# Performance work log

Measured on AMD Instinct MI355X. Metric: run time of the kernel, lower is better.

The kernel has to match this reference:

```python
import jax, jax.numpy as jnp
import numpy as np

EPS = 1e-5

def _bn(x, w, b, rm, rv):
    # eval-mode BatchNorm over channel axis (x: [..., C] broadcastable)
    return (x - rm) * (w * jax.lax.rsqrt(rv + EPS)) + b

def setup_inputs() -> dict:
    key = jax.random.key(0)
    ks = jax.random.split(key, 20)
    B, C, H, W = 2, 64, 96, 96
    Cq = C // 8  # query/key channels
    Cr = C // 8  # SE reduction channels
    s = 0.05
    inp = {
        'x': jax.random.normal(ks[0], (B, C, H, W), jnp.float32),
        'wq': jax.random.normal(ks[1], (Cq, C), jnp.float32) * s,
        'bq': jnp.zeros((Cq,), jnp.float32),
        'wk': jax.random.normal(ks[2], (Cq, C), jnp.float32) * s,
        'bk': jnp.zeros((Cq,), jnp.float32),
        'wv': jax.random.normal(ks[3], (C, C), jnp.float32) * s,
        'bv': jnp.zeros((C,), jnp.float32),
        'gamma': jnp.full((1,), 0.5, jnp.float32),
        'bn_w': jnp.ones((C,), jnp.float32),
        'bn_b': jnp.zeros((C,), jnp.float32),
        'bn_rm': jax.random.normal(ks[4], (C,), jnp.float32) * 0.1,
        'bn_rv': jax.random.uniform(ks[5], (C,), jnp.float32) + 0.5,
        'se_w1': jax.random.normal(ks[6], (Cr, C), jnp.float32) * s,
        'se_b1': jnp.zeros((Cr,), jnp.float32),
        'se_bn1_w': jnp.ones((Cr,), jnp.float32),
        'se_bn1_b': jnp.zeros((Cr,), jnp.float32),
        'se_bn1_rm': jax.random.normal(ks[7], (Cr,), jnp.float32) * 0.1,
        'se_bn1_rv': jax.random.uniform(ks[8], (Cr,), jnp.float32) + 0.5,
        'se_w2': jax.random.normal(ks[9], (C, Cr), jnp.float32) * s,
        'se_b2': jnp.zeros((C,), jnp.float32),
        'se_bn2_w': jnp.ones((C,), jnp.float32),
        'se_bn2_b': jnp.zeros((C,), jnp.float32),
        'se_bn2_rm': jax.random.normal(ks[10], (C,), jnp.float32) * 0.1,
        'se_bn2_rv': jax.random.uniform(ks[11], (C,), jnp.float32) + 0.5,
    }
    return inp

def reference(x, wq, bq, wk, bk, wv, bv, gamma, bn_w, bn_b, bn_rm, bn_rv,
              se_w1, se_b1, se_bn1_w, se_bn1_b, se_bn1_rm, se_bn1_rv,
              se_w2, se_b2, se_bn2_w, se_bn2_b, se_bn2_rm, se_bn2_rv):
    B, C, H, W = x.shape
    N = H * W
    xf = x.reshape(B, C, N)
    # PAM branch: 1x1 conv projections
    q = jnp.einsum('oc,bcn->bno', wq, xf) + bq            # [B,N,C/8]
    k = jnp.einsum('oc,bcn->bon', wk, xf) + bk[:, None]    # [B,C/8,N]
    v = jnp.einsum('oc,bcn->bon', wv, xf) + bv[:, None]    # [B,C,N]
    energy = jnp.einsum('bno,bom->bnm', q, k)              # [B,N,N]
    attn = jax.nn.softmax(energy, axis=-1)
    # out[b,c,i] = sum_j v[b,c,j] * attn[b,i,j]  (bmm(V, attn^T))
    out = jnp.einsum('bcj,bij->bci', v, attn)
    out = gamma[0] * out
    out = _bn(out, bn_w[:, None], bn_b[:, None], bn_rm[:, None], bn_rv[:, None])
    pam = out.reshape(B, C, H, W)
    # SE branch: GAP + 1x1 conv-bn-relu x2, multiplicative gate
    a = xf.mean(axis=2)                                    # [B,C]
    a1 = jax.nn.relu(_bn(a @ se_w1.T + se_b1, se_bn1_w, se_bn1_b, se_bn1_rm, se_bn1_rv))
    a2 = jax.nn.relu(_bn(a1 @ se_w2.T + se_b2, se_bn2_w, se_bn2_b, se_bn2_rm, se_bn2_rv))
    se = x * a2[:, :, None, None]
    return x + se + pam
```

## Files before the change

### kernel.cpp

```cpp
#include <hip/hip_runtime.h>
#include <hip/hip_bf16.h>

#define B_SZ   2
#define C_CH   64
#define NQ     8
#define NPIX   9216
#define NJC    288
#define QBLKS  288
#define KPART  4
#define KEYS_P 2304
#define NCHUNK 36
#define SM_F   2080
#define NP4    2304

typedef short bf16x8 __attribute__((ext_vector_type(8)));
typedef float f32x4  __attribute__((ext_vector_type(4)));
typedef unsigned u32x4 __attribute__((ext_vector_type(4)));
typedef unsigned uint2v __attribute__((ext_vector_type(2)));

static __device__ __forceinline__ unsigned pack2bf(float a, float b){
    union { __hip_bfloat16 h; unsigned short us; } ca, cb;
    ca.h = __float2bfloat16(a); cb.h = __float2bfloat16(b);
    return (unsigned)ca.us | ((unsigned)cb.us << 16);
}

static __device__ __forceinline__ unsigned short bf16b(float a){
    union { __hip_bfloat16 h; unsigned short us; } c;
    c.h = __float2bfloat16(a); return c.us;
}

__global__ __launch_bounds__(256) void prep_kernel(
    const float* __restrict__ x,
    const float* __restrict__ wq, const float* __restrict__ bq,
    const float* __restrict__ wk, const float* __restrict__ bk,
    const float* __restrict__ wv, const float* __restrict__ bv,
    __hip_bfloat16* __restrict__ qp, __hip_bfloat16* __restrict__ kp,
    __hip_bfloat16* __restrict__ vswz, float* __restrict__ amean)
{
    const int blk = blockIdx.x, tid = threadIdx.x;
    if (blk < 144){
        int t  = blk*256 + tid;
        int n  = (t % NP4) * 4;
        int c8 = (t / NP4) & 7;
        int b  = t / (NP4*8);
        c8 = __builtin_amdgcn_readfirstlane(c8);
        b  = __builtin_amdgcn_readfirstlane(b);
        float acc[8][4];
#pragma unroll
        for (int k = 0; k < 8; ++k){
            float bvv = bv[c8*8 + k];
            acc[k][0] = bvv; acc[k][1] = bvv; acc[k][2] = bvv; acc[k][3] = bvv;
        }
#pragma unroll 4
        for (int ci = 0; ci < C_CH; ++ci){
            const float4 xv = *reinterpret_cast<const float4*>(
                x + (size_t)(b*C_CH + ci)*NPIX + n);
#pragma unroll
            for (int k = 0; k < 8; ++k){
                float w = wv[(c8*8 + k)*C_CH + ci];
                acc[k][0] = fmaf(xv.x, w, acc[k][0]);
                acc[k][1] = fmaf(xv.y, w, acc[k][1]);
                acc[k][2] = fmaf(xv.z, w, acc[k][2]);
                acc[k][3] = fmaf(xv.w, w, acc[k][3]);
            }
        }
#pragma unroll
        for (int k = 0; k < 8; ++k){
            int c = c8*8 + k;
            size_t base = ((size_t)((b*NJC + (n >> 5))*4 + (c >> 4)))*512
                        + ((c & 15)*32) + (n & 31);
            unsigned long long wpk =
                (unsigned long long)pack2bf(acc[k][0], acc[k][1]) |
                ((unsigned long long)pack2bf(acc[k][2], acc[k][3]) << 32);
            *reinterpret_cast<unsigned long long*>(vswz + base) = wpk;
        }
    } else if (blk < 180){
        int t  = (blk - 144)*256 + tid;
        int n  = (t % NP4) * 4;
        int o8 = (t / NP4) & 1;
        int b  = t / (NP4*2);
        o8 = __builtin_amdgcn_readfirstlane(o8);
        b  = __builtin_amdgcn_readfirstlane(b);
        const bool isq = (o8 == 0);
        const float* w    = isq ? wq : wk;
        const float* bias = isq ? bq : bk;
        float acc[8][4];
#pragma unroll
        for (int k = 0; k < 8; ++k){
            float bb = bias[k];
            acc[k][0] = bb; acc[k][1] = bb; acc[k][2] = bb; acc[k][3] = bb;
        }
#pragma unroll 4
        for (int ci = 0; ci < C_CH; ++ci){
            const float4 xv = *reinterpret_cast<const float4*>(
                x + (size_t)(b*C_CH + ci)*NPIX + n);
#pragma unroll
            for (int k = 0; k < 8; ++k){
                float wv_ = w[k*C_CH + ci];
                acc[k][0] = fmaf(xv.x, wv_, acc[k][0]);
                acc[k][1] = fmaf(xv.y, wv_, acc[k][1]);
                acc[k][2] = fmaf(xv.z, wv_, acc[k][2]);
                acc[k][3] = fmaf(xv.w, wv_, acc[k][3]);
            }
        }
        if (isq){
#pragma unroll
            for (int k = 0; k < 8; ++k)
#pragma unroll
                for (int px = 0; px < 4; ++px) acc[k][px] *= 1.44269504f;
        }
        __hip_bfloat16* dst = isq ? qp : kp;
#pragma unroll
        for (int px = 0; px < 4; ++px){
            bf16x8 row;
#pragma unroll
            for (int k = 0; k < 8; ++k) row[k] = (short)bf16b(acc[k][px]);
            *reinterpret_cast<bf16x8*>(dst + ((size_t)(b*NPIX + n + px))*NQ) = row;
        }
    } else {
        int bc = blk - 180;
        float s = 0.f;
        for (int i = tid; i < NPIX; i += 256) s += x[(size_t)bc*NPIX + i];
#pragma unroll
        for (int o = 32; o > 0; o >>= 1) s += __shfl_down(s, o, 64);
        __shared__ float red[4];
        if ((tid & 63) == 0) red[tid >> 6] = s;
        __syncthreads();
        if (tid == 0) amean[bc] = (red[0] + red[1] + red[2] + red[3]) * (1.f / (float)NPIX);
    }
}

__global__ __launch_bounds__(256, 4) void flash_fused(
    const __hip_bfloat16* __restrict__ qp,
    const __hip_bfloat16* __restrict__ kp,
    const __hip_bfloat16* __restrict__ vswz,
    const float* __restrict__ amean,
    const float* __restrict__ sw1, const float* __restrict__ sb1,
    const float* __restrict__ s1w, const float* __restrict__ s1b,
    const float* __restrict__ s1m, const float* __restrict__ s1v,
    const float* __restrict__ sw2, const float* __restrict__ sb2,
    const float* __restrict__ s2w, const float* __restrict__ s2b,
    const float* __restrict__ s2m, const float* __restrict__ s2v,
    const float* __restrict__ x,
    const float* __restrict__ gamma,
    const float* __restrict__ bnw, const float* __restrict__ bnb,
    const float* __restrict__ bnm, const float* __restrict__ bnv,
    float* __restrict__ out)
{
    __shared__ __align__(16) float sm[KPART*SM_F];

    const int qt2 = blockIdx.x, b = blockIdx.y;
    const int p  = threadIdx.x >> 6;
    const int l  = threadIdx.x & 63;
    const int lq = l & 15;
    const int lg = l >> 4;
    const int vlane = lq*32 + lg*8;

    float a1r;
    {
        int r8 = l & 7;
        float s = sb1[r8];
#pragma unroll 8
        for (int c = 0; c < C_CH; ++c)
            s = fmaf(amean[b*C_CH + c], sw1[r8*C_CH + c], s);
        s = (s - s1m[r8]) * (s1w[r8] * rsqrtf(s1v[r8] + 1e-5f)) + s1b[r8];
        a1r = fmaxf(s, 0.f);
    }

    bf16x8 zf = {0,0,0,0,0,0,0,0};
    bf16x8 qfrag[2];
#pragma unroll
    for (int qi = 0; qi < 2; ++qi){
        qfrag[qi] = zf;
        if (lg == 0)
            qfrag[qi] = *reinterpret_cast<const bf16x8*>(
                qp + (size_t)(b*NPIX + qt2*32 + qi*16 + lq) * NQ);
    }

    bf16x8 ones;
#pragma unroll
    for (int i = 0; i < 8; ++i) ones[i] = (short)0x3F80;

    f32x4 Of[2][4];
#pragma unroll
    for (int qi = 0; qi < 2; ++qi)
#pragma unroll
        for (int i = 0; i < 4; ++i) Of[qi][i] = (f32x4){0.f, 0.f, 0.f, 0.f};
    f32x4 Lf[2];
    Lf[0] = (f32x4){0.f, 0.f, 0.f, 0.f};
    Lf[1] = (f32x4){0.f, 0.f, 0.f, 0.f};

    for (int ch = 0; ch < NCHUNK; ++ch){
        const int j0  = p*KEYS_P + ch*64;
        const int jcb = b*NJC + (j0 >> 5);

        bf16x8 kf[4];
#pragma unroll
        for (int jt = 0; jt < 4; ++jt){
            kf[jt] = zf;
            if (lg == 0)
                kf[jt] = *reinterpret_cast<const bf16x8*>(kp + (size_t)(b*NPIX + j0 + jt*16 + lq) * NQ);
        }
        bf16x8 vf[2][4];
#pragma unroll
        for (int kc = 0; kc < 2; ++kc)
#pragma unroll
            for (int ct = 0; ct < 4; ++ct)
                vf[kc][ct] = *reinterpret_cast<const bf16x8*>(
                    vswz + ((size_t)((jcb + kc)*4 + ct))*512 + vlane);

#pragma unroll
        for (int qi = 0; qi < 2; ++qi){
            f32x4 Sf[4];
#pragma unroll
            for (int jt = 0; jt < 4; ++jt)
                Sf[jt] = __builtin_amdgcn_mfma_f32_16x16x32_bf16(kf[jt], qfrag[qi], (f32x4){0.f,0.f,0.f,0.f}, 0, 0, 0);

            unsigned D[4][2];
#pragma unroll
            for (int jt = 0; jt < 4; ++jt){
                D[jt][0] = pack2bf(exp2f(Sf[jt][0]), exp2f(Sf[jt][1]));
                D[jt][1] = pack2bf(exp2f(Sf[jt][2]), exp2f(Sf[jt][3]));
            }

#pragma unroll
            for (int kc = 0; kc < 2; ++kc){
                unsigned o0, o1, o2, o3;
                {
                    uint2v r1 = __builtin_amdgcn_permlane32_swap(D[2*kc][0], D[2*kc+1][0], false, false);
                    uint2v r2 = __builtin_amdgcn_permlane16_swap(r1[0], r1[1], false, false);
                    o0 = r2[0]; o2 = r2[1];
                }
                {
                    uint2v r1 = __builtin_amdgcn_permlane32_swap(D[2*kc][1], D[2*kc+1][1], false, false);
                    uint2v r2 = __builtin_amdgcn_permlane16_swap(r1[0], r1[1], false, false);
                    o1 = r2[0]; o3 = r2[1];
                }
                u32x4 pu; pu[0] = o0; pu[1] = o1; pu[2] = o2; pu[3] = o3;
                bf16x8 pf = __builtin_bit_cast(bf16x8, pu);
#pragma unroll
                for (int ct = 0; ct < 4; ++ct)
                    Of[qi][ct] = __builtin_amdgcn_mfma_f32_16x16x32_bf16(vf[kc][ct], pf, Of[qi][ct], 0, 0, 0);
                Lf[qi] = __builtin_amdgcn_mfma_f32_16x16x32_bf16(ones, pf, Lf[qi], 0, 0, 0);
            }
        }
    }

#pragma unroll
    for (int qi = 0; qi < 2; ++qi)
#pragma unroll
        for (int ct = 0; ct < 4; ++ct)
#pragma unroll
            for (int r = 0; r < 4; ++r)
                sm[p*SM_F + qi*1024 + (ct*4 + r)*64 + l] = Of[qi][ct][r];
    if (l < 16){
        sm[p*SM_F + 2048 + lq]      = Lf[0][0];
        sm[p*SM_F + 2048 + 16 + lq] = Lf[1][0];
    }
    __syncthreads();

    {
        const int ct = threadIdx.x >> 6;
        float gam = gamma[0];

        float a1g[8];
#pragma unroll
        for (int j = 0; j < 8; ++j) a1g[j] = __shfl(a1r, (l & 56) | j, 64);
        float a2v[4];
#pragma unroll
        for (int r = 0; r < 4; ++r){
            int c = ct*16 + lg*4 + r;
            float s = sb2[c];
#pragma unroll
            for (int j = 0; j < 8; ++j) s = fmaf(a1g[j], sw2[c*NQ + j], s);
            s = (s - s2m[c]) * (s2w[c] * rsqrtf(s2v[c] + 1e-5f)) + s2b[c];
            a2v[r] = fmaxf(s, 0.f);
        }

#pragma unroll
        for (int qi = 0; qi < 2; ++qi){
            float L = 0.f;
#pragma unroll
            for (int q = 0; q < KPART; ++q) L += sm[q*SM_F + 2048 + qi*16 + lq];
            float invL = 1.f / L;
            int n = qt2*32 + qi*16 + lq;
#pragma unroll
            for (int r = 0; r < 4; ++r){
                float O = 0.f;
#pragma unroll
                for (int q = 0; q < KPART; ++q) O += sm[q*SM_F + qi*1024 + (ct*4 + r)*64 + l];
                int c = ct*16 + lg*4 + r;
                float pam = gam * O * invL;
                pam = (pam - bnm[c]) * (bnw[c] * rsqrtf(bnv[c] + 1e-5f)) + bnb[c];
                float xv = x[(size_t)(b*C_CH + c)*NPIX + n];
                out[(size_t)(b*C_CH + c)*NPIX + n] = fmaf(xv, a2v[r], xv + pam);
            }
        }
    }
}

extern "C" void kernel_launch(void* const* d_in, const int* in_sizes, int n_in,
                              void* d_out, int out_size, void* d_ws, size_t ws_size,
                              hipStream_t stream)
{
    const float* x     = (const float*)d_in[0];
    const float* wq    = (const float*)d_in[1];
    const float* bq    = (const float*)d_in[2];
    const float* wk    = (const float*)d_in[3];
    const float* bk    = (const float*)d_in[4];
    const float* wv    = (const float*)d_in[5];
    const float* bv    = (const float*)d_in[6];
    const float* gamma = (const float*)d_in[7];
    const float* bnw   = (const float*)d_in[8];
    const float* bnb   = (const float*)d_in[9];
    const float* bnm   = (const float*)d_in[10];
    const float* bnv   = (const float*)d_in[11];
    const float* sw1   = (const float*)d_in[12];
    const float* sb1   = (const float*)d_in[13];
    const float* s1w   = (const float*)d_in[14];
    const float* s1b   = (const float*)d_in[15];
    const float* s1m   = (const float*)d_in[16];
    const float* s1v   = (const float*)d_in[17];
    const float* sw2   = (const float*)d_in[18];
    const float* sb2   = (const float*)d_in[19];
    const float* s2w   = (const float*)d_in[20];
    const float* s2b   = (const float*)d_in[21];
    const float* s2m   = (const float*)d_in[22];
    const float* s2v   = (const float*)d_in[23];

    size_t off = 0;
    auto give = [&](size_t bytes) -> void* {
        void* r = (char*)d_ws + off;
        off += (bytes + 255) & ~(size_t)255;
        return r;
    };
    __hip_bfloat16* qp   = (__hip_bfloat16*)give((size_t)B_SZ*NPIX*NQ*2);
    __hip_bfloat16* kp   = (__hip_bfloat16*)give((size_t)B_SZ*NPIX*NQ*2);
    __hip_bfloat16* vswz = (__hip_bfloat16*)give((size_t)B_SZ*C_CH*NPIX*2);
    float* amean = (float*)give((size_t)B_SZ*C_CH*4);

    prep_kernel<<<dim3(308), dim3(256), 0, stream>>>(x, wq, bq, wk, bk, wv, bv,
                                                     qp, kp, vswz, amean);
    flash_fused<<<dim3(QBLKS, B_SZ), dim3(256), 0, stream>>>(
        qp, kp, vswz, amean,
        sw1, sb1, s1w, s1b, s1m, s1v,
        sw2, sb2, s2w, s2b, s2m, s2v,
        x, gamma, bnw, bnb, bnm, bnv, (float*)d_out);
}
```

Before: 212.9 us.

## Split keys across eight waves per block with two-stage LDS reduction

Doubles the waves per flash block from four to eight, so each wave handles half as many keys (1152 instead of 2304). The partial O and L accumulators are combined in two steps: the upper four waves write to shared memory, then the lower four add into it. This keeps the shared-memory footprint at four slices. The epilogue is re-split so each of the eight waves handles one (query half, channel tile) pair. The aim is more latency hiding and shorter per-wave serial chains, at the cost of an extra barrier and an LDS read-modify-write. Launch bounds of 512x4 may also constrain registers and cause spills.

```diff
diff --git a/kernel.cpp b/kernel.cpp
--- a/kernel.cpp
+++ b/kernel.cpp
@@ -7,9 +7,9 @@
 #define NPIX   9216
 #define NJC    288
 #define QBLKS  288
-#define KPART  4
-#define KEYS_P 2304
-#define NCHUNK 36
+#define KPART  8
+#define KEYS_P 1152
+#define NCHUNK 18
 #define SM_F   2080
 #define NP4    2304
 
@@ -130,7 +130,7 @@
     }
 }
 
-__global__ __launch_bounds__(256, 4) void flash_fused(
+__global__ __launch_bounds__(512, 4) void flash_fused(
     const __hip_bfloat16* __restrict__ qp,
     const __hip_bfloat16* __restrict__ kp,
     const __hip_bfloat16* __restrict__ vswz,
@@ -147,7 +147,7 @@
     const float* __restrict__ bnm, const float* __restrict__ bnv,
     float* __restrict__ out)
 {
-    __shared__ __align__(16) float sm[KPART*SM_F];
+    __shared__ __align__(16) float sm[4*SM_F];
 
     const int qt2 = blockIdx.x, b = blockIdx.y;
     const int p  = threadIdx.x >> 6;
@@ -246,21 +246,40 @@
         }
     }
 
-#pragma unroll
-    for (int qi = 0; qi < 2; ++qi)
-#pragma unroll
-        for (int ct = 0; ct < 4; ++ct)
-#pragma unroll
-            for (int r = 0; r < 4; ++r)
-                sm[p*SM_F + qi*1024 + (ct*4 + r)*64 + l] = Of[qi][ct][r];
-    if (l < 16){
-        sm[p*SM_F + 2048 + lq]      = Lf[0][0];
-        sm[p*SM_F + 2048 + 16 + lq] = Lf[1][0];
+    if (p >= 4){
+        const int ps = p - 4;
+#pragma unroll
+        for (int qi = 0; qi < 2; ++qi)
+#pragma unroll
+            for (int ct = 0; ct < 4; ++ct)
+#pragma unroll
+                for (int r = 0; r < 4; ++r)
+                    sm[ps*SM_F + qi*1024 + (ct*4 + r)*64 + l] = Of[qi][ct][r];
+        if (l < 16){
+            sm[ps*SM_F + 2048 + lq]      = Lf[0][0];
+            sm[ps*SM_F + 2048 + 16 + lq] = Lf[1][0];
+        }
     }
     __syncthreads();
+    if (p < 4){
+#pragma unroll
+        for (int qi = 0; qi < 2; ++qi)
+#pragma unroll
+            for (int ct = 0; ct < 4; ++ct)
+#pragma unroll
+                for (int r = 0; r < 4; ++r)
+                    sm[p*SM_F + qi*1024 + (ct*4 + r)*64 + l] += Of[qi][ct][r];
+        if (l < 16){
+            sm[p*SM_F + 2048 + lq]      += Lf[0][0];
+            sm[p*SM_F + 2048 + 16 + lq] += Lf[1][0];
+        }
+    }
+    __syncthreads();
 
     {
-        const int ct = threadIdx.x >> 6;
+        const int w8 = threadIdx.x >> 6;
+        const int qi = w8 >> 2;
+        const int ct = w8 & 3;
         float gam = gamma[0];
 
         float a1g[8];
@@ -277,24 +296,21 @@
             a2v[r] = fmaxf(s, 0.f);
         }
 
-#pragma unroll
-        for (int qi = 0; qi < 2; ++qi){
-            float L = 0.f;
-#pragma unroll
-            for (int q = 0; q < KPART; ++q) L += sm[q*SM_F + 2048 + qi*16 + lq];
-            float invL = 1.f / L;
-            int n = qt2*32 + qi*16 + lq;
-#pragma unroll
-            for (int r = 0; r < 4; ++r){
-                float O = 0.f;
-#pragma unroll
-                for (int q = 0; q < KPART; ++q) O += sm[q*SM_F + qi*1024 + (ct*4 + r)*64 + l];
-                int c = ct*16 + lg*4 + r;
-                float pam = gam * O * invL;
-                pam = (pam - bnm[c]) * (bnw[c] * rsqrtf(bnv[c] + 1e-5f)) + bnb[c];
-                float xv = x[(size_t)(b*C_CH + c)*NPIX + n];
-                out[(size_t)(b*C_CH + c)*NPIX + n] = fmaf(xv, a2v[r], xv + pam);
-            }
+        float L = 0.f;
+#pragma unroll
+        for (int q = 0; q < 4; ++q) L += sm[q*SM_F + 2048 + qi*16 + lq];
+        float invL = 1.f / L;
+        int n = qt2*32 + qi*16 + lq;
+#pragma unroll
+        for (int r = 0; r < 4; ++r){
+            float O = 0.f;
+#pragma unroll
+            for (int q = 0; q < 4; ++q) O += sm[q*SM_F + qi*1024 + (ct*4 + r)*64 + l];
+            int c = ct*16 + lg*4 + r;
+            float pam = gam * O * invL;
+            pam = (pam - bnm[c]) * (bnw[c] * rsqrtf(bnv[c] + 1e-5f)) + bnb[c];
+            float xv = x[(size_t)(b*C_CH + c)*NPIX + n];
+            out[(size_t)(b*C_CH + c)*NPIX + n] = fmaf(xv, a2v[r], xv + pam);
         }
     }
 }
@@ -341,7 +357,7 @@
 
     prep_kernel<<<dim3(308), dim3(256), 0, stream>>>(x, wq, bq, wk, bk, wv, bv,
                                                      qp, kp, vswz, amean);
-    flash_fused<<<dim3(QBLKS, B_SZ), dim3(256), 0, stream>>>(
+    flash_fused<<<dim3(QBLKS, B_SZ), dim3(512), 0, stream>>>(
         qp, kp, vswz, amean,
         sw1, sb1, s1w, s1b, s1m, s1v,
         sw2, sb2, s2w, s2b, s2m, s2v,
```

Measured after the change: 211.7 us. About the same (-0.5%).
